# Kernel optimization log

Hardware: AMD Instinct MI355X
Metric: run time of the kernel (lower is better)

The kernel has to match this reference:

```python
import jax, jax.numpy as jnp
import numpy as np

B, N, NE = 16, 96, 256
ATOM, EDIM, HID, LAT, HEADS = 128, 16, 128, 128, 4
HD = LAT // HEADS
RBF, CUT, ZEMB, MAXZ = 16, 5.0, 32, 100
MUL0_IN, MUL1_IN = 64, 32      # irreps_node = 64x0e + 32x1o (dim 160)
MUL0_OUT, MUL1_OUT = 32, 16    # out irreps  = 32x0e + 16x1o (dim 80)
NODE_DIM = MUL0_IN + 3 * MUL1_IN
OUT_DIM = MUL0_OUT + 3 * MUL1_OUT
E_ATT = 1024
WNUM = MUL0_IN*MUL0_OUT + MUL0_IN*MUL1_OUT + MUL1_IN*MUL1_OUT + MUL1_IN*MUL0_OUT  # 4608


def _mlp3(x, w1, b1, w2, b2, w3, b3):
    x = jax.nn.silu(x @ w1 + b1)
    x = jax.nn.silu(x @ w2 + b2)
    return x @ w3 + b3


def setup_inputs() -> dict:
    key = jax.random.key(0)
    ks = jax.random.split(key, 40)
    s = 0.05  # scale params so deep MLP activations stay numerically sane
    d = {}
    d['h'] = jax.random.normal(ks[0], (B, N, ATOM), jnp.float32)
    d['h_full'] = jax.random.normal(ks[1], (B, N, NODE_DIM), jnp.float32)
    d['e_feat'] = jax.random.normal(ks[2], (NE, EDIM), jnp.float32)
    d['att_dist'] = jax.random.uniform(ks[3], (E_ATT,), jnp.float32)
    d['att_vec'] = jax.random.normal(ks[4], (E_ATT, 3), jnp.float32)
    d['z_emb_table'] = jax.random.normal(ks[5], (MAXZ + 1, ZEMB), jnp.float32) * s
    d['rw1'] = jax.random.normal(ks[6], (ZEMB + 1 + RBF, HID), jnp.float32) * s
    d['rb1'] = jnp.zeros((HID,), jnp.float32)
    d['rw2'] = jax.random.normal(ks[7], (HID, WNUM), jnp.float32) * s
    d['rb2'] = jnp.zeros((WNUM,), jnp.float32)
    d['ew1'] = jax.random.normal(ks[8], (EDIM, HID), jnp.float32) * s
    d['eb1'] = jnp.zeros((HID,), jnp.float32)
    d['ew2'] = jax.random.normal(ks[9], (HID, MUL0_OUT + MUL1_OUT), jnp.float32) * s
    d['eb2'] = jnp.zeros((MUL0_OUT + MUL1_OUT,), jnp.float32)
    d['qw1'] = jax.random.normal(ks[10], (ATOM + EDIM, HID), jnp.float32) * s
    d['qb1'] = jnp.zeros((HID,), jnp.float32)
    d['qw2'] = jax.random.normal(ks[11], (HID, HID), jnp.float32) * s
    d['qb2'] = jnp.zeros((HID,), jnp.float32)
    d['qw3'] = jax.random.normal(ks[12], (HID, LAT), jnp.float32) * s
    d['qb3'] = jnp.zeros((LAT,), jnp.float32)
    d['kw1'] = jax.random.normal(ks[13], (ATOM + ZEMB + 1 + RBF, HID), jnp.float32) * s
    d['kb1'] = jnp.zeros((HID,), jnp.float32)
    d['kw2'] = jax.random.normal(ks[14], (HID, HID), jnp.float32) * s
    d['kb2'] = jnp.zeros((HID,), jnp.float32)
    d['kw3'] = jax.random.normal(ks[15], (HID, LAT), jnp.float32) * s
    d['kb3'] = jnp.zeros((LAT,), jnp.float32)
    d['ow1'] = jax.random.normal(ks[16], (MUL0_OUT + MUL1_OUT, HID), jnp.float32) * s
    d['ob1'] = jnp.zeros((HID,), jnp.float32)
    d['ow2'] = jax.random.normal(ks[17], (HID, HID), jnp.float32) * s
    d['ob2'] = jnp.zeros((HID,), jnp.float32)
    d['ow3'] = jax.random.normal(ks[18], (HID, LAT), jnp.float32) * s
    d['ob3'] = jnp.zeros((LAT,), jnp.float32)
    d['z'] = jax.random.randint(ks[19], (B, N), 0, MAXZ)
    d['mask'] = jnp.ones((B, N), bool)
    d['absorber_index'] = jax.random.randint(ks[20], (B,), 0, N)
    d['att_dst'] = jnp.arange(E_ATT)  # unique flat indices into B*N
    return d


def reference(h, h_full, e_feat, att_dist, att_vec, z_emb_table,
              rw1, rb1, rw2, rb2, ew1, eb1, ew2, eb2,
              qw1, qb1, qw2, qb2, qw3, qb3,
              kw1, kb1, kw2, kb2, kw3, kb3,
              ow1, ob1, ow2, ob2, ow3, ob3,
              z, mask, absorber_index, att_dst):
    Bz, Na, Hd = h.shape
    F = Bz * Na
    nE = e_feat.shape[0]
    # scatter edge data into flat (B*N) atom slots
    am_flat = jnp.zeros((F,), bool).at[att_dst].set(True)
    d_flat = jnp.zeros((F,), h.dtype).at[att_dst].set(att_dist)
    v_flat = jnp.zeros((F, 3), h.dtype).at[att_dst].set(att_vec)
    att_mask = am_flat.reshape(Bz, Na) & mask
    # spherical harmonics (lmax=1, component normalization): Y0 = 1, Y1 = sqrt(3)*unit_vec
    un = v_flat / jnp.maximum(jnp.linalg.norm(v_flat, axis=-1, keepdims=True), 1e-8)
    y1 = jnp.sqrt(3.0) * un
    # Gaussian RBF on absorber->atom distance
    mu = jnp.linspace(0.0, CUT, RBF)
    delta = CUT / (RBF - 1)
    rbf = jnp.exp(-(d_flat[:, None] - mu) ** 2 / (2.0 * delta * delta))  # (F, RBF)
    zr = z_emb_table[z]                      # (B, N, ZEMB)
    zr_flat = zr.reshape(F, -1)
    is_abs = jnp.zeros((Bz, Na), h.dtype).at[jnp.arange(Bz), absorber_index].set(1.0)
    # radial MLP -> per-edge tensor-product weights
    w_in = jnp.concatenate([zr_flat, is_abs.reshape(F, 1), rbf], -1)
    tpw = jax.nn.silu(w_in @ rw1 + rb1) @ rw2 + rb2  # (F, WNUM)
    s1 = MUL0_IN * MUL0_OUT
    s2 = s1 + MUL0_IN * MUL1_OUT
    s3 = s2 + MUL1_IN * MUL1_OUT
    w00 = tpw[:, :s1].reshape(F, MUL0_IN, MUL0_OUT)   # 0e x 0e -> 0e
    w01 = tpw[:, s1:s2].reshape(F, MUL0_IN, MUL1_OUT) # 0e x 1o -> 1o
    w10 = tpw[:, s2:s3].reshape(F, MUL1_IN, MUL1_OUT) # 1o x 0e -> 1o
    w11 = tpw[:, s3:].reshape(F, MUL1_IN, MUL0_OUT)   # 1o x 1o -> 0e
    hf = h_full.reshape(F, -1)
    x0 = hf[:, :MUL0_IN]
    x1 = hf[:, MUL0_IN:].reshape(F, MUL1_IN, 3)
    alpha = 1.0 / jnp.sqrt(jnp.float32(MUL0_IN + MUL1_IN))  # path fan-in normalization
    c = 1.0 / jnp.sqrt(3.0)                                  # wigner-3j coeff for l=1 couplings
    out0 = alpha * (jnp.einsum('fi,fio->fo', x0, w00)
                    + c * jnp.einsum('fim,fm,fio->fo', x1, y1, w11))
    out1 = alpha * c * (jnp.einsum('fi,fm,fio->fom', x0, y1, w01)
                        + jnp.einsum('fim,fio->fom', x1, w10))
    v_irrep = jnp.concatenate([out0, out1.reshape(F, 3 * MUL1_OUT)], -1)  # (F, OUT_DIM)
    # cosine cutoff envelope + edge mask
    env = jnp.where(d_flat < CUT, 0.5 * (jnp.cos(jnp.pi * d_flat / CUT) + 1.0), 0.0)
    v_irrep = v_irrep * (am_flat.astype(h.dtype) * env)[:, None]
    # energy-conditioned per-irrep-channel modulation
    gates = jax.nn.silu(e_feat @ ew1 + eb1) @ ew2 + eb2  # (nE, 48)
    g_exp = jnp.concatenate([gates[:, :MUL0_OUT],
                             jnp.repeat(gates[:, MUL0_OUT:], 3, axis=-1)], -1)  # (nE, OUT_DIM)
    v_mod = (v_irrep[:, None, :] * g_exp[None]).reshape(Bz, Na, nE, OUT_DIM)
    # invariant multi-head scoring
    h_abs = h[jnp.arange(Bz), absorber_index]  # (B, H)
    q_in = jnp.concatenate([jnp.broadcast_to(h_abs[:, None], (Bz, nE, Hd)),
                            jnp.broadcast_to(e_feat[None], (Bz, nE, EDIM))], -1)
    q = _mlp3(q_in, qw1, qb1, qw2, qb2, qw3, qb3)  # (B, nE, LAT)
    atom_static = jnp.concatenate([h, zr, is_abs[..., None], rbf.reshape(Bz, Na, RBF)], -1)
    k = _mlp3(atom_static, kw1, kb1, kw2, kb2, kw3, kb3)  # (B, N, LAT)
    qh = q.reshape(Bz, nE, HEADS, HD)
    kh = k.reshape(Bz, Na, HEADS, HD)
    scores = (jnp.einsum('behd,bnhd->benh', qh, kh) * (HD ** -0.5)).mean(-1)  # (B, nE, N)
    m = att_mask[:, None, :]
    scores = jnp.where(m, scores, -1e9)
    attn = jax.nn.softmax(scores, axis=2) * m.astype(h.dtype)
    attn = attn / jnp.maximum(attn.sum(2, keepdims=True), 1e-8)
    out_irrep = jnp.einsum('ben,bnec->bec', attn, v_mod)  # (B, nE, OUT_DIM)
    # invariants: scalars + vector norms
    scal = out_irrep[..., :MUL0_OUT]
    vec = out_irrep[..., MUL0_OUT:].reshape(Bz, nE, MUL1_OUT, 3)
    inv = jnp.concatenate([scal, jnp.sqrt(jnp.sum(vec * vec, -1) + 1e-12)], -1)
    return _mlp3(inv, ow1, ob1, ow2, ob2, ow3, ob3)  # (B, nE, LAT)
```

## Files before the change

kernel.cpp:

```cpp
#include <hip/hip_runtime.h>
#include <hip/hip_fp16.h>
#include <math.h>

#define BB 16
#define NN 96
#define NE 256
#define FF (BB*NN)
#define ATOM 128
#define EDIM 16
#define HID 128
#define LAT 128
#define RBFN 16
#define CUTOFF 5.0f
#define ZEMB 32
#define E_ATT 1024
#define M0I 64
#define M1I 32
#define M0O 32
#define M1O 16
#define NODE_DIM 160
#define OUT_DIM 80
#define INVD 48
#define WNUM 4608
#define SEG1 2048
#define SEG2 3072
#define SEG3 3584

#define NODE_BLKS (FF/4)
#define EC_BLKS 16
#define HABS_BLKS 2
#define GATE_BLKS 16
#define STAGE1_BLKS (NODE_BLKS + EC_BLKS + HABS_BLKS + GATE_BLKS)

#define MFMA_BLKS (36*16)
#define MQ_BLKS (MFMA_BLKS + 512)

typedef _Float16 half8_t __attribute__((ext_vector_type(8)));
typedef float float4v __attribute__((ext_vector_type(4)));

__device__ __forceinline__ float silu_f(float x) { return x / (1.0f + expf(-x)); }

__global__ __launch_bounds__(256) void k_prep(
    const float* __restrict__ rw2,
    const int* __restrict__ att_dst, const float* __restrict__ att_dist,
    const float* __restrict__ att_vec,
    __half* __restrict__ rw2T, int* __restrict__ inv,
    float* __restrict__ y1E, float* __restrict__ envE)
{
    int blk = blockIdx.x;
    int t = threadIdx.x;
    if (blk < 144) {
        __shared__ __half lds[64][66];
        int nt = blk % 72, kt = blk / 72;
        int n0 = nt*64, k0 = kt*64;
        for (int p = 0; p < 16; p++) {
            int idx = t + 256*p;
            int kk = idx >> 6, nn = idx & 63;
            lds[nn][kk] = __float2half(rw2[(k0+kk)*WNUM + n0+nn]);
        }
        __syncthreads();
        for (int p = 0; p < 16; p++) {
            int idx = t + 256*p;
            int nn = idx >> 6, kk = idx & 63;
            rw2T[(n0+nn)*HID + k0+kk] = lds[nn][kk];
        }
        return;
    }
    for (int p = 0; p < 6; p++) inv[t + 256*p] = -1;
    for (int p = 0; p < 4; p++) {
        int e = t + 256*p;
        float d = att_dist[e];
        envE[e] = (d < CUTOFF) ? 0.5f*(cosf(3.14159265358979323846f*d/CUTOFF) + 1.0f) : 0.0f;
        float vx = att_vec[3*e], vy = att_vec[3*e+1], vz = att_vec[3*e+2];
        float nrm = sqrtf(vx*vx + vy*vy + vz*vz);
        float is = 1.0f / fmaxf(nrm, 1e-8f);
        const float s3 = 1.7320508075688772f;
        y1E[3*e]   = s3*vx*is;
        y1E[3*e+1] = s3*vy*is;
        y1E[3*e+2] = s3*vz*is;
    }
    __syncthreads();
    for (int p = 0; p < 4; p++) { int e = t + 256*p; inv[att_dst[e]] = e; }
}

__global__ __launch_bounds__(256) void k_stage1(
    const float* __restrict__ h, const float* __restrict__ z_emb, const int* __restrict__ z,
    const int* __restrict__ absorber, const float* __restrict__ e_feat,
    const int* __restrict__ inv, const float* __restrict__ att_dist,
    const float* __restrict__ rw1, const float* __restrict__ rb1,
    const float* __restrict__ kw1, const float* __restrict__ kb1,
    const float* __restrict__ kw2, const float* __restrict__ kb2,
    const float* __restrict__ kw3, const float* __restrict__ kb3,
    const float* __restrict__ qw1,
    const float* __restrict__ ew1, const float* __restrict__ eb1,
    const float* __restrict__ ew2, const float* __restrict__ eb2,
    __half* __restrict__ hiddenH, float* __restrict__ kmatw,
    float* __restrict__ ecw, float* __restrict__ habs1w, float* __restrict__ gexp)
{
    __shared__ float smem[3488];
    int blk = blockIdx.x;
    int t = threadIdx.x;

    if (blk < NODE_BLKS) {
        float (*sin1)[184] = (float(*)[184])smem;
        float (*l1S)[128]  = (float(*)[128])(smem + 736);
        float (*l2S)[128]  = (float(*)[128])(smem + 736 + 512);
        int f0 = blk * 4;
        {
            int n = t >> 6, i2 = t & 63;
            float2 hv = *(const float2*)&h[(f0 + n)*ATOM + i2*2];
            sin1[n][i2*2] = hv.x; sin1[n][i2*2 + 1] = hv.y;
        }
        if (t < 128) {
            int n = t >> 5, j = t & 31;
            sin1[n][ATOM + j] = z_emb[z[f0 + n]*ZEMB + j];
        }
        if (t < 64) {
            int n = t >> 4, j = t & 15;
            int e = inv[f0 + n];
            float d = ((unsigned)e < E_ATT) ? att_dist[e] : 0.0f;
            const float delta = CUTOFF / (RBFN - 1);
            float diff = d - j*delta;
            sin1[n][ATOM + ZEMB + 1 + j] = expf(-diff*diff / (2.0f*delta*delta));
        }
        if (t < 4) {
            int f = f0 + t;
            int b = f / NN, nn = f - b*NN;
            sin1[t][ATOM + ZEMB] = (absorber[b] == nn) ? 1.0f : 0.0f;
        }
        __syncthreads();
        int n = t >> 6;
        int c2 = (t & 63) * 2;
        int e = inv[f0 + n];
        bool att_ = ((unsigned)e < E_ATT);
        if (att_) {
            float2 a0 = *(const float2*)&rb1[c2];
            float2 a1 = make_float2(0.f, 0.f);
            #pragma unroll 8
            for (int i = 0; i < 48; i += 2) {
                float x0v = sin1[n][ATOM + i], x1v = sin1[n][ATOM + i + 1];
                float2 w0 = *(const float2*)&rw1[i*HID + c2];
                float2 w1 = *(const float2*)&rw1[(i+1)*HID + c2];
                a0.x += x0v*w0.x; a0.y += x0v*w0.y;
                a1.x += x1v*w1.x; a1.y += x1v*w1.y;
            }
            {
                float x0v = sin1[n][ATOM + 48];
                float2 w0 = *(const float2*)&rw1[48*HID + c2];
                a0.x += x0v*w0.x; a0.y += x0v*w0.y;
            }
            *(__half2*)&hiddenH[e*HID + c2] =
                __floats2half2_rn(silu_f(a0.x + a1.x), silu_f(a0.y + a1.y));
        }
        {
            float2 a0 = *(const float2*)&kb1[c2];
            float2 a1 = make_float2(0.f, 0.f);
            #pragma unroll 8
            for (int i = 0; i < 176; i += 2) {
                float x0v = sin1[n][i], x1v = sin1[n][i + 1];
                float2 w0 = *(const float2*)&kw1[i*HID + c2];
                float2 w1 = *(const float2*)&kw1[(i+1)*HID + c2];
                a0.x += x0v*w0.x; a0.y += x0v*w0.y;
                a1.x += x1v*w1.x; a1.y += x1v*w1.y;
            }
            {
                float x0v = sin1[n][176];
                float2 w0 = *(const float2*)&kw1[176*HID + c2];
                a0.x += x0v*w0.x; a0.y += x0v*w0.y;
            }
            l1S[n][c2] = silu_f(a0.x + a1.x); l1S[n][c2+1] = silu_f(a0.y + a1.y);
        }
        __syncthreads();
        {
            float2 a0 = *(const float2*)&kb2[c2];
            float2 a1 = make_float2(0.f, 0.f);
            #pragma unroll 8
            for (int i = 0; i < HID; i += 2) {
                float x0v = l1S[n][i], x1v = l1S[n][i + 1];
                float2 w0 = *(const float2*)&kw2[i*HID + c2];
                float2 w1 = *(const float2*)&kw2[(i+1)*HID + c2];
                a0.x += x0v*w0.x; a0.y += x0v*w0.y;
                a1.x += x1v*w1.x; a1.y += x1v*w1.y;
            }
            l2S[n][c2] = silu_f(a0.x + a1.x); l2S[n][c2+1] = silu_f(a0.y + a1.y);
        }
        __syncthreads();
        {
            float2 a0 = *(const float2*)&kb3[c2];
            float2 a1 = make_float2(0.f, 0.f);
            #pragma unroll 8
            for (int i = 0; i < HID; i += 2) {
                float x0v = l2S[n][i], x1v = l2S[n][i + 1];
                float2 w0 = *(const float2*)&kw3[i*HID + c2];
                float2 w1 = *(const float2*)&kw3[(i+1)*HID + c2];
                a0.x += x0v*w0.x; a0.y += x0v*w0.y;
                a1.x += x1v*w1.x; a1.y += x1v*w1.y;
            }
            float2 o; o.x = a0.x + a1.x; o.y = a0.y + a1.y;
            *(float2*)&kmatw[(f0 + n)*HID + c2] = o;
        }
    } else if (blk < NODE_BLKS + EC_BLKS) {
        float (*ef)[16] = (float(*)[16])smem;
        int e0 = (blk - NODE_BLKS) * 16;
        { int e = t >> 4, i = t & 15; ef[e][i] = e_feat[(e0 + e)*EDIM + i]; }
        __syncthreads();
        int r = t >> 4, c0 = (t & 15)*8;
        float4 a0 = make_float4(0,0,0,0), a1 = a0;
        #pragma unroll
        for (int i = 0; i < EDIM; i++) {
            float a = ef[r][i];
            float4 w0 = *(const float4*)&qw1[(ATOM + i)*HID + c0];
            float4 w1 = *(const float4*)&qw1[(ATOM + i)*HID + c0 + 4];
            a0.x += a*w0.x; a0.y += a*w0.y; a0.z += a*w0.z; a0.w += a*w0.w;
            a1.x += a*w1.x; a1.y += a*w1.y; a1.z += a*w1.z; a1.w += a*w1.w;
        }
        *(float4*)&ecw[(e0 + r)*HID + c0] = a0;
        *(float4*)&ecw[(e0 + r)*HID + c0 + 4] = a1;
    } else if (blk < NODE_BLKS + EC_BLKS + HABS_BLKS) {
        float (*hr)[128] = (float(*)[128])smem;
        int b0 = (blk - NODE_BLKS - EC_BLKS) * 8;
        {
            int r = t >> 5, i4 = t & 31;
            int b = b0 + r;
            int a = absorber[b];
            *(float4*)&hr[r][i4*4] = *(const float4*)&h[(b*NN + a)*ATOM + i4*4];
        }
        __syncthreads();
        int r = t >> 5, c0 = (t & 31)*4;
        float4 a0 = make_float4(0,0,0,0), a1 = a0;
        #pragma unroll 8
        for (int i = 0; i < ATOM; i += 2) {
            float x0v = hr[r][i], x1v = hr[r][i+1];
            float4 w0 = *(const float4*)&qw1[i*HID + c0];
            float4 w1 = *(const float4*)&qw1[(i+1)*HID + c0];
            a0.x += x0v*w0.x; a0.y += x0v*w0.y; a0.z += x0v*w0.z; a0.w += x0v*w0.w;
            a1.x += x1v*w1.x; a1.y += x1v*w1.y; a1.z += x1v*w1.z; a1.w += x1v*w1.w;
        }
        float4 o;
        o.x = a0.x + a1.x; o.y = a0.y + a1.y; o.z = a0.z + a1.z; o.w = a0.w + a1.w;
        *(float4*)&habs1w[(b0 + r)*HID + c0] = o;
    } else {
        float (*ef)[16]   = (float(*)[16])smem;
        float (*l1g)[128] = (float(*)[128])(smem + 256);
        float (*gg)[48]   = (float(*)[48])(smem + 256 + 2048);
        int e0 = (blk - NODE_BLKS - EC_BLKS - HABS_BLKS) * 16;
        { int e = t >> 4, i = t & 15; ef[e][i] = e_feat[(e0 + e)*EDIM + i]; }
        __syncthreads();
        int r = t >> 4, c0 = (t & 15)*8;
        {
            float4 a0 = *(const float4*)&eb1[c0];
            float4 a1 = *(const float4*)&eb1[c0 + 4];
            #pragma unroll
            for (int i = 0; i < EDIM; i++) {
                float a = ef[r][i];
                float4 w0 = *(const float4*)&ew1[i*HID + c0];
                float4 w1 = *(const float4*)&ew1[i*HID + c0 + 4];
                a0.x += a*w0.x; a0.y += a*w0.y; a0.z += a*w0.z; a0.w += a*w0.w;
                a1.x += a*w1.x; a1.y += a*w1.y; a1.z += a*w1.z; a1.w += a*w1.w;
            }
            l1g[r][c0]   = silu_f(a0.x); l1g[r][c0+1] = silu_f(a0.y);
            l1g[r][c0+2] = silu_f(a0.z); l1g[r][c0+3] = silu_f(a0.w);
            l1g[r][c0+4] = silu_f(a1.x); l1g[r][c0+5] = silu_f(a1.y);
            l1g[r][c0+6] = silu_f(a1.z); l1g[r][c0+7] = silu_f(a1.w);
        }
        __syncthreads();
        for (int u = t; u < 16*48; u += 256) {
            int e = u / 48, j = u - 48*(u/48);
            float acc = eb2[j];
            #pragma unroll 4
            for (int i = 0; i < HID; i++) acc += l1g[e][i]*ew2[i*48 + j];
            gg[e][j] = acc;
        }
        __syncthreads();
        for (int u = t; u < 16*80; u += 256) {
            int e = u / 80, cc = u - 80*(u/80);
            gexp[(e0 + e)*OUT_DIM + cc] = (cc < M0O) ? gg[e][cc] : gg[e][M0O + (cc - M0O)/3];
        }
    }
}

__global__ __launch_bounds__(256) void k_mq(
    const __half* __restrict__ hiddenH, const __half* __restrict__ rw2T,
    const float* __restrict__ rb2,
    const float* __restrict__ habs1, const float* __restrict__ ec, const float* __restrict__ qb1,
    const float* __restrict__ qw2, const float* __restrict__ qb2,
    const float* __restrict__ qw3, const float* __restrict__ qb3,
    __half* __restrict__ tpwE, float* __restrict__ qmat)
{
    __shared__ float smem[2048];
    int blk = blockIdx.x;
    int t = threadIdx.x;
    if (blk < MFMA_BLKS) {
        int colTile = blk % 36;
        int rowGrp  = blk / 36;
        int wv = t >> 6;
        int lane = t & 63;
        int m0 = (rowGrp*4 + wv) * 16;
        int n0 = colTile * 128;
        int mrow = lane & 15, quad = lane >> 4;
        const _Float16* hp = (const _Float16*)hiddenH + (m0 + mrow)*HID + quad*8;
        half8_t af[4];
        #pragma unroll
        for (int kc = 0; kc < 4; kc++) af[kc] = *(const half8_t*)(hp + kc*32);
        #pragma unroll
        for (int nt = 0; nt < 8; nt++) {
            const _Float16* bp = (const _Float16*)rw2T + (n0 + nt*16 + mrow)*HID + quad*8;
            float4v acc = {0.f, 0.f, 0.f, 0.f};
            #pragma unroll
            for (int kc = 0; kc < 4; kc++) {
                half8_t bf = *(const half8_t*)(bp + kc*32);
                acc = __builtin_amdgcn_mfma_f32_16x16x32_f16(af[kc], bf, acc, 0, 0, 0);
            }
            int col = n0 + nt*16 + mrow;
            float bias = rb2[col];
            int rbase = m0 + quad*4;
            #pragma unroll
            for (int r = 0; r < 4; r++)
                tpwE[(long)(rbase + r)*WNUM + col] = __float2half(acc[r] + bias);
        }
    } else {
        float* l1S = smem;
        float* l2S = smem + 1024;
        int r0 = (blk - MFMA_BLKS) * 8;
        for (int p = 0; p < 4; p++) {
            int idx = t + 256*p;
            int rr = idx >> 7, i = idx & 127;
            int be = r0 + rr; int b = be >> 8; int e = be & 255;
            l1S[rr*128 + i] = silu_f(habs1[b*HID + i] + ec[e*HID + i] + qb1[i]);
        }
        __syncthreads();
        int r = t >> 5, c0 = (t & 31)*4;
        {
            float4 a0 = *(const float4*)&qb2[c0];
            float4 a1 = make_float4(0,0,0,0);
            #pragma unroll 8
            for (int i = 0; i < HID; i += 2) {
                float x0v = l1S[r*128 + i], x1v = l1S[r*128 + i+1];
                float4 w0 = *(const float4*)&qw2[i*HID + c0];
                float4 w1 = *(const float4*)&qw2[(i+1)*HID + c0];
                a0.x += x0v*w0.x; a0.y += x0v*w0.y; a0.z += x0v*w0.z; a0.w += x0v*w0.w;
                a1.x += x1v*w1.x; a1.y += x1v*w1.y; a1.z += x1v*w1.z; a1.w += x1v*w1.w;
            }
            l2S[r*128 + c0]   = silu_f(a0.x + a1.x); l2S[r*128 + c0+1] = silu_f(a0.y + a1.y);
            l2S[r*128 + c0+2] = silu_f(a0.z + a1.z); l2S[r*128 + c0+3] = silu_f(a0.w + a1.w);
        }
        __syncthreads();
        {
            float4 a0 = *(const float4*)&qb3[c0];
            float4 a1 = make_float4(0,0,0,0);
            #pragma unroll 8
            for (int i = 0; i < HID; i += 2) {
                float x0v = l2S[r*128 + i], x1v = l2S[r*128 + i+1];
                float4 w0 = *(const float4*)&qw3[i*HID + c0];
                float4 w1 = *(const float4*)&qw3[(i+1)*HID + c0];
                a0.x += x0v*w0.x; a0.y += x0v*w0.y; a0.z += x0v*w0.z; a0.w += x0v*w0.w;
                a1.x += x1v*w1.x; a1.y += x1v*w1.y; a1.z += x1v*w1.z; a1.w += x1v*w1.w;
            }
            float4 o;
            o.x = a0.x + a1.x; o.y = a0.y + a1.y; o.z = a0.z + a1.z; o.w = a0.w + a1.w;
            *(float4*)&qmat[(r0 + r)*LAT + c0] = o;
        }
    }
}

__global__ __launch_bounds__(256) void k_score(
    const float* __restrict__ qmat, const float* __restrict__ kmat, const int* __restrict__ inv,
    float* __restrict__ scoresW)
{
    int b  = blockIdx.x >> 3;
    int e0 = (blockIdx.x & 7) * 32;
    int t = threadIdx.x;
    __shared__ float Qs[32][132];
    __shared__ float Ks[96][132];
    __shared__ float mS[NN];

    for (int p = 0; p < 4; p++) {
        int idx = t + 256*p; int e = idx >> 5, i4 = idx & 31;
        *(float4*)&Qs[e][i4*4] = *(const float4*)&qmat[(b*NE + e0 + e)*LAT + i4*4];
    }
    for (int p = 0; p < 12; p++) {
        int idx = t + 256*p; int n = idx >> 5, i4 = idx & 31;
        *(float4*)&Ks[n][i4*4] = *(const float4*)&kmat[(b*NN + n)*LAT + i4*4];
    }
    if (t < NN) mS[t] = ((unsigned)inv[b*NN + t] < E_ATT) ? 1.0f : 0.0f;
    __syncthreads();

    int te = t >> 5;
    int tn = t & 31;
    float acc[4][3] = {};
    for (int i = 0; i < LAT; i++) {
        float bv0 = Ks[tn][i], bv1 = Ks[tn + 32][i], bv2 = Ks[tn + 64][i];
        #pragma unroll
        for (int j = 0; j < 4; j++) {
            float a = Qs[te*4 + j][i];
            acc[j][0] += a*bv0; acc[j][1] += a*bv1; acc[j][2] += a*bv2;
        }
    }
    const float scale = 0.04419417382415922f;
    #pragma unroll
    for (int j = 0; j < 4; j++)
        #pragma unroll
        for (int jj = 0; jj < 3; jj++) {
            int n = tn + 32*jj;
            float s = (mS[n] != 0.f) ? acc[j][jj]*scale : -1e9f;
            scoresW[((b*NE) + e0 + te*4 + j)*NN + n] = s;
        }
}

__global__ __launch_bounds__(256) void k_attf(
    const float* __restrict__ scoresW, const int* __restrict__ inv,
    const float* __restrict__ virr, const float* __restrict__ gexp,
    const float* __restrict__ ow1, const float* __restrict__ ob1,
    const float* __restrict__ ow2, const float* __restrict__ ob2,
    const float* __restrict__ ow3, const float* __restrict__ ob3,
    float* __restrict__ out)
{
    int b  = blockIdx.x >> 5;
    int e0 = (blockIdx.x & 31) * 8;
    int t = threadIdx.x;
    __shared__ float aS[8][100];
    __shared__ float gS[8][84];
    __shared__ float ocS[8][84];
    __shared__ float mS[NN];
    __shared__ float inS[8][INVD];
    __shared__ float l1S[8][HID];
    __shared__ float l2S[8][HID];

    for (int p = 0; p < 3; p++) {
        int idx = t + 256*p;
        int el = idx / NN, n = idx - NN*(idx/NN);
        aS[el][n] = scoresW[((b*NE) + e0 + el)*NN + n];
    }
    if (t < 160) {
        int el = t / 20, c4 = t - 20*(t/20);
        *(float4*)&gS[el][c4*4] = *(const float4*)&gexp[(e0 + el)*OUT_DIM + c4*4];
    }
    if (t < NN) mS[t] = ((unsigned)inv[b*NN + t] < E_ATT) ? 1.0f : 0.0f;
    __syncthreads();

    {
        int el = t >> 5;
        int ng = t & 31;
        float s0 = aS[el][ng], s1 = aS[el][ng + 32], s2 = aS[el][ng + 64];
        float m0 = mS[ng], m1 = mS[ng + 32], m2 = mS[ng + 64];
        float mx = fmaxf(s0, fmaxf(s1, s2));
        #pragma unroll
        for (int off = 1; off < 32; off <<= 1) mx = fmaxf(mx, __shfl_xor(mx, off));
        float e0v = expf(s0 - mx), e1v = expf(s1 - mx), e2v = expf(s2 - mx);
        float sm = e0v + e1v + e2v;
        #pragma unroll
        for (int off = 1; off < 32; off <<= 1) sm += __shfl_xor(sm, off);
        float r = 1.0f / sm;
        float p0 = m0*e0v*r, p1 = m1*e1v*r, p2 = m2*e2v*r;
        float ss = p0 + p1 + p2;
        #pragma unroll
        for (int off = 1; off < 32; off <<= 1) ss += __shfl_xor(ss, off);
        float is = 1.0f / fmaxf(ss, 1e-8f);
        aS[el][ng]      = p0*is;
        aS[el][ng + 32] = p1*is;
        aS[el][ng + 64] = p2*is;
    }
    __syncthreads();

    if (t < 160) {
        int el = t / 20, c4 = t - 20*(t/20);
        const float* vp = virr + (long)b*NN*OUT_DIM + c4*4;
        float4 acc = make_float4(0,0,0,0);
        #pragma unroll 4
        for (int n = 0; n < NN; n++) {
            float a = aS[el][n];
            float4 v = *(const float4*)&vp[n*OUT_DIM];
            acc.x += a*v.x; acc.y += a*v.y; acc.z += a*v.z; acc.w += a*v.w;
        }
        float4 g = *(float4*)&gS[el][c4*4];
        float4 o; o.x = acc.x*g.x; o.y = acc.y*g.y; o.z = acc.z*g.z; o.w = acc.w*g.w;
        *(float4*)&ocS[el][c4*4] = o;
    }
    __syncthreads();

    for (int u = t; u < 8*INVD; u += 256) {
        int el = u / INVD, j = u - INVD*(u/INVD);
        float val;
        if (j < M0O) val = ocS[el][j];
        else {
            int o = j - M0O;
            float x = ocS[el][M0O + 3*o], y = ocS[el][M0O + 3*o + 1], zz = ocS[el][M0O + 3*o + 2];
            val = sqrtf(x*x + y*y + zz*zz + 1e-12f);
        }
        inS[el][j] = val;
    }
    __syncthreads();

    int r = t >> 5, c0 = (t & 31)*4;
    {
        float4 a0 = *(const float4*)&ob1[c0];
        float4 a1 = make_float4(0,0,0,0);
        #pragma unroll 8
        for (int i = 0; i < INVD; i += 2) {
            float x0v = inS[r][i], x1v = inS[r][i+1];
            float4 w0 = *(const float4*)&ow1[i*HID + c0];
            float4 w1 = *(const float4*)&ow1[(i+1)*HID + c0];
            a0.x += x0v*w0.x; a0.y += x0v*w0.y; a0.z += x0v*w0.z; a0.w += x0v*w0.w;
            a1.x += x1v*w1.x; a1.y += x1v*w1.y; a1.z += x1v*w1.z; a1.w += x1v*w1.w;
        }
        l1S[r][c0]   = silu_f(a0.x + a1.x); l1S[r][c0+1] = silu_f(a0.y + a1.y);
        l1S[r][c0+2] = silu_f(a0.z + a1.z); l1S[r][c0+3] = silu_f(a0.w + a1.w);
    }
    __syncthreads();
    {
        float4 a0 = *(const float4*)&ob2[c0];
        float4 a1 = make_float4(0,0,0,0);
        #pragma unroll 8
        for (int i = 0; i < HID; i += 2) {
            float x0v = l1S[r][i], x1v = l1S[r][i+1];
            float4 w0 = *(const float4*)&ow2[i*HID + c0];
            float4 w1 = *(const float4*)&ow2[(i+1)*HID + c0];
            a0.x += x0v*w0.x; a0.y += x0v*w0.y; a0.z += x0v*w0.z; a0.w += x0v*w0.w;
            a1.x += x1v*w1.x; a1.y += x1v*w1.y; a1.z += x1v*w1.z; a1.w += x1v*w1.w;
        }
        l2S[r][c0]   = silu_f(a0.x + a1.x); l2S[r][c0+1] = silu_f(a0.y + a1.y);
        l2S[r][c0+2] = silu_f(a0.z + a1.z); l2S[r][c0+3] = silu_f(a0.w + a1.w);
    }
    __syncthreads();
    {
        float4 a0 = *(const float4*)&ob3[c0];
        float4 a1 = make_float4(0,0,0,0);
        #pragma unroll 8
        for (int i = 0; i < HID; i += 2) {
            float x0v = l2S[r][i], x1v = l2S[r][i+1];
            float4 w0 = *(const float4*)&ow3[i*HID + c0];
            float4 w1 = *(const float4*)&ow3[(i+1)*HID + c0];
            a0.x += x0v*w0.x; a0.y += x0v*w0.y; a0.z += x0v*w0.z; a0.w += x0v*w0.w;
            a1.x += x1v*w1.x; a1.y += x1v*w1.y; a1.z += x1v*w1.z; a1.w += x1v*w1.w;
        }
        float4 o;
        o.x = a0.x + a1.x; o.y = a0.y + a1.y; o.z = a0.z + a1.z; o.w = a0.w + a1.w;
        *(float4*)&out[((b*NE + e0) + r)*LAT + c0] = o;
    }
}

__global__ __launch_bounds__(128) void k_tp(
    const float* __restrict__ h_full, const __half* __restrict__ tpwE,
    const int* __restrict__ att_dst,
    const float* __restrict__ envE, const float* __restrict__ y1E,
    float* __restrict__ virr)
{
    int e = blockIdx.x; int t = threadIdx.x;
    int f = att_dst[e];
    __shared__ float x0[M0I];
    __shared__ float x1f[M1I*3];
    __shared__ float xy[M1I];
    __shared__ float y1s[3];
    const float* hf = h_full + f*NODE_DIM;
    if (t < M0I) x0[t] = hf[t];
    if (t < M1I*3) x1f[t] = hf[M0I + t];
    if (t < 3) y1s[t] = y1E[3*e + t];
    __syncthreads();
    if (t < M1I) xy[t] = x1f[3*t]*y1s[0] + x1f[3*t+1]*y1s[1] + x1f[3*t+2]*y1s[2];
    __syncthreads();
    float scale = envE[e];
    const __half* w = tpwE + (long)e*WNUM;
    const float alpha = 0.10206207261596575f;
    const float cc = 0.5773502691896258f;
    if (t < M0O) {
        float t00 = 0.f, t11 = 0.f;
        #pragma unroll 4
        for (int i = 0; i < M0I; i++) t00 += x0[i]*__half2float(w[i*M0O + t]);
        #pragma unroll 4
        for (int i = 0; i < M1I; i++) t11 += xy[i]*__half2float(w[SEG3 + i*M0O + t]);
        virr[f*OUT_DIM + t] = alpha*(t00 + cc*t11)*scale;
    } else if (t < M0O + 3*M1O) {
        int idx = t - M0O; int o = idx/3, m = idx - 3*o;
        float t01 = 0.f, t10 = 0.f;
        #pragma unroll 4
        for (int i = 0; i < M0I; i++) t01 += x0[i]*__half2float(w[SEG1 + i*M1O + o]);
        #pragma unroll 4
        for (int i = 0; i < M1I; i++) t10 += x1f[i*3 + m]*__half2float(w[SEG2 + i*M1O + o]);
        virr[f*OUT_DIM + t] = alpha*cc*(t01*y1s[m] + t10)*scale;
    }
}

extern "C" void kernel_launch(void* const* d_in, const int* in_sizes, int n_in,
                              void* d_out, int out_size, void* d_ws, size_t ws_size,
                              hipStream_t stream) {
    const float* h        = (const float*)d_in[0];
    const float* h_full   = (const float*)d_in[1];
    const float* e_feat   = (const float*)d_in[2];
    const float* att_dist = (const float*)d_in[3];
    const float* att_vec  = (const float*)d_in[4];
    const float* z_emb    = (const float*)d_in[5];
    const float* rw1 = (const float*)d_in[6];  const float* rb1 = (const float*)d_in[7];
    const float* rw2 = (const float*)d_in[8];  const float* rb2 = (const float*)d_in[9];
    const float* ew1 = (const float*)d_in[10]; const float* eb1 = (const float*)d_in[11];
    const float* ew2 = (const float*)d_in[12]; const float* eb2 = (const float*)d_in[13];
    const float* qw1 = (const float*)d_in[14]; const float* qb1 = (const float*)d_in[15];
    const float* qw2 = (const float*)d_in[16]; const float* qb2 = (const float*)d_in[17];
    const float* qw3 = (const float*)d_in[18]; const float* qb3 = (const float*)d_in[19];
    const float* kw1 = (const float*)d_in[20]; const float* kb1 = (const float*)d_in[21];
    const float* kw2 = (const float*)d_in[22]; const float* kb2 = (const float*)d_in[23];
    const float* kw3 = (const float*)d_in[24]; const float* kb3 = (const float*)d_in[25];
    const float* ow1 = (const float*)d_in[26]; const float* ob1 = (const float*)d_in[27];
    const float* ow2 = (const float*)d_in[28]; const float* ob2 = (const float*)d_in[29];
    const float* ow3 = (const float*)d_in[30]; const float* ob3 = (const float*)d_in[31];
    const int* z        = (const int*)d_in[32];
    const int* absorber = (const int*)d_in[34];
    const int* att_dst  = (const int*)d_in[35];

    float* ws = (float*)d_ws;
    int*   inv     = (int*)ws;
    float* y1E     = ws + 1536;
    float* envE    = ws + 4608;
    float* kmat    = ws + 5632;
    float* qmat    = ws + 202240;
    float* gexp    = ws + 726528;
    float* virr    = ws + 747008;
    float* habs1   = ws + 869888;
    float* ec      = ws + 871936;
    float* scoresW = ws + 904704;
    __half* tpwE   = (__half*)(ws + 1297920);
    __half* rw2T   = (__half*)(ws + 3657216);
    __half* hiddenH= (__half*)(ws + 3952128);

    float* out = (float*)d_out;

    k_prep<<<145, 256, 0, stream>>>(rw2, att_dst, att_dist, att_vec, rw2T, inv, y1E, envE);
    k_stage1<<<STAGE1_BLKS, 256, 0, stream>>>(h, z_emb, z, absorber, e_feat, inv, att_dist,
                                              rw1, rb1, kw1, kb1, kw2, kb2, kw3, kb3,
                                              qw1, ew1, eb1, ew2, eb2,
                                              hiddenH, kmat, ec, habs1, gexp);
    k_mq<<<MQ_BLKS, 256, 0, stream>>>(hiddenH, rw2T, rb2, habs1, ec, qb1,
                                      qw2, qb2, qw3, qb3, tpwE, qmat);
    k_score<<<128, 256, 0, stream>>>(qmat, kmat, inv, scoresW);
    k_tp<<<E_ATT, 128, 0, stream>>>(h_full, tpwE, att_dst, envE, y1E, virr);
    k_attf<<<BB*32, 256, 0, stream>>>(scoresW, inv, virr, gexp,
                                      ow1, ob1, ow2, ob2, ow3, ob3, out);
}
```

Baseline: 250.5 us.

## Move rw2 transpose into stage1, stage MFMA output via LDS, pack tp blocks

The rw2 fp16 transpose moves out of k_prep into extra blocks of k_stage1, so it runs alongside the node MLP work. k_prep shrinks to a single 1024-thread block. The MFMA epilogue in k_mq now stages each 16x128 tile in LDS and writes tpwE rows as 16-byte vectors instead of scattered 2-byte stores. k_tp processes two edges per 256-thread block. Together these aim to cut launch and serialization overhead and uncoalesced global writes, at the cost of more LDS use in k_mq.

Result: no change. 248.4 us (-0.8%).

```diff
diff --git a/kernel.cpp b/kernel.cpp
--- a/kernel.cpp
+++ b/kernel.cpp
@@ -30,7 +30,8 @@
 #define EC_BLKS 16
 #define HABS_BLKS 2
 #define GATE_BLKS 16
-#define STAGE1_BLKS (NODE_BLKS + EC_BLKS + HABS_BLKS + GATE_BLKS)
+#define TRANS_BLKS 144
+#define STAGE1_BLKS (NODE_BLKS + EC_BLKS + HABS_BLKS + GATE_BLKS + TRANS_BLKS)
 
 #define MFMA_BLKS (36*16)
 #define MQ_BLKS (MFMA_BLKS + 512)
@@ -40,47 +41,27 @@
 
 __device__ __forceinline__ float silu_f(float x) { return x / (1.0f + expf(-x)); }
 
-__global__ __launch_bounds__(256) void k_prep(
-    const float* __restrict__ rw2,
+__global__ __launch_bounds__(1024) void k_prep(
     const int* __restrict__ att_dst, const float* __restrict__ att_dist,
     const float* __restrict__ att_vec,
-    __half* __restrict__ rw2T, int* __restrict__ inv,
-    float* __restrict__ y1E, float* __restrict__ envE)
+    int* __restrict__ inv, float* __restrict__ y1E, float* __restrict__ envE)
 {
-    int blk = blockIdx.x;
     int t = threadIdx.x;
-    if (blk < 144) {
-        __shared__ __half lds[64][66];
-        int nt = blk % 72, kt = blk / 72;
-        int n0 = nt*64, k0 = kt*64;
-        for (int p = 0; p < 16; p++) {
-            int idx = t + 256*p;
-            int kk = idx >> 6, nn = idx & 63;
-            lds[nn][kk] = __float2half(rw2[(k0+kk)*WNUM + n0+nn]);
-        }
-        __syncthreads();
-        for (int p = 0; p < 16; p++) {
-            int idx = t + 256*p;
-            int nn = idx >> 6, kk = idx & 63;
-            rw2T[(n0+nn)*HID + k0+kk] = lds[nn][kk];
-        }
-        return;
-    }
-    for (int p = 0; p < 6; p++) inv[t + 256*p] = -1;
-    for (int p = 0; p < 4; p++) {
-        int e = t + 256*p;
-        float d = att_dist[e];
-        envE[e] = (d < CUTOFF) ? 0.5f*(cosf(3.14159265358979323846f*d/CUTOFF) + 1.0f) : 0.0f;
-        float vx = att_vec[3*e], vy = att_vec[3*e+1], vz = att_vec[3*e+2];
+    inv[t] = -1;
+    if (t < FF - 1024) inv[1024 + t] = -1;
+    {
+        float d = att_dist[t];
+        envE[t] = (d < CUTOFF) ? 0.5f*(cosf(3.14159265358979323846f*d/CUTOFF) + 1.0f) : 0.0f;
+        float vx = att_vec[3*t], vy = att_vec[3*t+1], vz = att_vec[3*t+2];
         float nrm = sqrtf(vx*vx + vy*vy + vz*vz);
         float is = 1.0f / fmaxf(nrm, 1e-8f);
         const float s3 = 1.7320508075688772f;
-        y1E[3*e]   = s3*vx*is;
-        y1E[3*e+1] = s3*vy*is;
-        y1E[3*e+2] = s3*vz*is;
-    }
-    __syncthreads();
-    for (int p = 0; p < 4; p++) { int e = t + 256*p; inv[att_dst[e]] = e; }
+        y1E[3*t]   = s3*vx*is;
+        y1E[3*t+1] = s3*vy*is;
+        y1E[3*t+2] = s3*vz*is;
+    }
+    __syncthreads();
+    inv[att_dst[t]] = t;
 }
 
 __global__ __launch_bounds__(256) void k_stage1(
@@ -94,8 +75,10 @@
     const float* __restrict__ qw1,
     const float* __restrict__ ew1, const float* __restrict__ eb1,
     const float* __restrict__ ew2, const float* __restrict__ eb2,
+    const float* __restrict__ rw2,
     __half* __restrict__ hiddenH, float* __restrict__ kmatw,
-    float* __restrict__ ecw, float* __restrict__ habs1w, float* __restrict__ gexp)
+    float* __restrict__ ecw, float* __restrict__ habs1w, float* __restrict__ gexp,
+    __half* __restrict__ rw2T)
 {
     __shared__ float smem[3488];
     int blk = blockIdx.x;
@@ -239,7 +222,7 @@
         float4 o;
         o.x = a0.x + a1.x; o.y = a0.y + a1.y; o.z = a0.z + a1.z; o.w = a0.w + a1.w;
         *(float4*)&habs1w[(b0 + r)*HID + c0] = o;
-    } else {
+    } else if (blk < NODE_BLKS + EC_BLKS + HABS_BLKS + GATE_BLKS) {
         float (*ef)[16]   = (float(*)[16])smem;
         float (*l1g)[128] = (float(*)[128])(smem + 256);
         float (*gg)[48]   = (float(*)[48])(smem + 256 + 2048);
@@ -276,6 +259,22 @@
             int e = u / 80, cc = u - 80*(u/80);
             gexp[(e0 + e)*OUT_DIM + cc] = (cc < M0O) ? gg[e][cc] : gg[e][M0O + (cc - M0O)/3];
         }
+    } else {
+        __half* lds = (__half*)smem;
+        int tb = blk - (NODE_BLKS + EC_BLKS + HABS_BLKS + GATE_BLKS);
+        int nt = tb % 72, kt = tb / 72;
+        int n0 = nt*64, k0 = kt*64;
+        for (int p = 0; p < 16; p++) {
+            int idx = t + 256*p;
+            int kk = idx >> 6, nn = idx & 63;
+            lds[nn*66 + kk] = __float2half(rw2[(k0+kk)*WNUM + n0+nn]);
+        }
+        __syncthreads();
+        for (int p = 0; p < 16; p++) {
+            int idx = t + 256*p;
+            int nn = idx >> 6, kk = idx & 63;
+            rw2T[(n0+nn)*HID + k0+kk] = lds[nn*66 + kk];
+        }
     }
 }
 
@@ -287,7 +286,7 @@
     const float* __restrict__ qw3, const float* __restrict__ qb3,
     __half* __restrict__ tpwE, float* __restrict__ qmat)
 {
-    __shared__ float smem[2048];
+    __shared__ __align__(16) char smemraw[17408];
     int blk = blockIdx.x;
     int t = threadIdx.x;
     if (blk < MFMA_BLKS) {
@@ -298,6 +297,7 @@
         int m0 = (rowGrp*4 + wv) * 16;
         int n0 = colTile * 128;
         int mrow = lane & 15, quad = lane >> 4;
+        __half* cS = (__half*)smemraw + wv * (16*136);
         const _Float16* hp = (const _Float16*)hiddenH + (m0 + mrow)*HID + quad*8;
         half8_t af[4];
         #pragma unroll
@@ -311,16 +311,21 @@
                 half8_t bf = *(const half8_t*)(bp + kc*32);
                 acc = __builtin_amdgcn_mfma_f32_16x16x32_f16(af[kc], bf, acc, 0, 0, 0);
             }
-            int col = n0 + nt*16 + mrow;
-            float bias = rb2[col];
-            int rbase = m0 + quad*4;
+            float bias = rb2[n0 + nt*16 + mrow];
             #pragma unroll
             for (int r = 0; r < 4; r++)
-                tpwE[(long)(rbase + r)*WNUM + col] = __float2half(acc[r] + bias);
+                cS[(quad*4 + r)*136 + nt*16 + mrow] = __float2half(acc[r] + bias);
+        }
+        #pragma unroll
+        for (int p = 0; p < 4; p++) {
+            int chunk = lane + 64*p;
+            int row = chunk >> 4, c8 = (chunk & 15)*8;
+            float4 v = *(float4*)&cS[row*136 + c8];
+            *(float4*)&tpwE[(long)(m0 + row)*WNUM + n0 + c8] = v;
         }
     } else {
-        float* l1S = smem;
-        float* l2S = smem + 1024;
+        float* l1S = (float*)smemraw;
+        float* l2S = (float*)smemraw + 1024;
         int r0 = (blk - MFMA_BLKS) * 8;
         for (int p = 0; p < 4; p++) {
             int idx = t + 256*p;
@@ -405,6 +410,50 @@
             float s = (mS[n] != 0.f) ? acc[j][jj]*scale : -1e9f;
             scoresW[((b*NE) + e0 + te*4 + j)*NN + n] = s;
         }
+}
+
+__global__ __launch_bounds__(256) void k_tp(
+    const float* __restrict__ h_full, const __half* __restrict__ tpwE,
+    const int* __restrict__ att_dst,
+    const float* __restrict__ envE, const float* __restrict__ y1E,
+    float* __restrict__ virr)
+{
+    int t = threadIdx.x;
+    int sub = t >> 7, tt = t & 127;
+    int e = blockIdx.x*2 + sub;
+    int f = att_dst[e];
+    __shared__ float x0[2][M0I];
+    __shared__ float x1f[2][M1I*3];
+    __shared__ float xy[2][M1I];
+    __shared__ float y1s[2][3];
+    const float* hf = h_full + f*NODE_DIM;
+    if (tt < M0I) x0[sub][tt] = hf[tt];
+    if (tt < M1I*3) x1f[sub][tt] = hf[M0I + tt];
+    if (tt < 3) y1s[sub][tt] = y1E[3*e + tt];
+    __syncthreads();
+    if (tt < M1I) xy[sub][tt] = x1f[sub][3*tt]*y1s[sub][0] + x1f[sub][3*tt+1]*y1s[sub][1]
+                              + x1f[sub][3*tt+2]*y1s[sub][2];
+    __syncthreads();
+    float scale = envE[e];
+    const __half* w = tpwE + (long)e*WNUM;
+    const float alpha = 0.10206207261596575f;
+    const float cc = 0.5773502691896258f;
+    if (tt < M0O) {
+        float t00 = 0.f, t11 = 0.f;
+        #pragma unroll 4
+        for (int i = 0; i < M0I; i++) t00 += x0[sub][i]*__half2float(w[i*M0O + tt]);
+        #pragma unroll 4
+        for (int i = 0; i < M1I; i++) t11 += xy[sub][i]*__half2float(w[SEG3 + i*M0O + tt]);
+        virr[f*OUT_DIM + tt] = alpha*(t00 + cc*t11)*scale;
+    } else if (tt < M0O + 3*M1O) {
+        int idx = tt - M0O; int o = idx/3, m = idx - 3*o;
+        float t01 = 0.f, t10 = 0.f;
+        #pragma unroll 4
+        for (int i = 0; i < M0I; i++) t01 += x0[sub][i]*__half2float(w[SEG1 + i*M1O + o]);
+        #pragma unroll 4
+        for (int i = 0; i < M1I; i++) t10 += x1f[sub][i*3 + m]*__half2float(w[SEG2 + i*M1O + o]);
+        virr[f*OUT_DIM + tt] = alpha*cc*(t01*y1s[sub][m] + t10)*scale;
+    }
 }
 
 __global__ __launch_bounds__(256) void k_attf(
@@ -536,47 +585,6 @@
         float4 o;
         o.x = a0.x + a1.x; o.y = a0.y + a1.y; o.z = a0.z + a1.z; o.w = a0.w + a1.w;
         *(float4*)&out[((b*NE + e0) + r)*LAT + c0] = o;
-    }
-}
-
-__global__ __launch_bounds__(128) void k_tp(
-    const float* __restrict__ h_full, const __half* __restrict__ tpwE,
-    const int* __restrict__ att_dst,
-    const float* __restrict__ envE, const float* __restrict__ y1E,
-    float* __restrict__ virr)
-{
-    int e = blockIdx.x; int t = threadIdx.x;
-    int f = att_dst[e];
-    __shared__ float x0[M0I];
-    __shared__ float x1f[M1I*3];
-    __shared__ float xy[M1I];
-    __shared__ float y1s[3];
-    const float* hf = h_full + f*NODE_DIM;
-    if (t < M0I) x0[t] = hf[t];
-    if (t < M1I*3) x1f[t] = hf[M0I + t];
-    if (t < 3) y1s[t] = y1E[3*e + t];
-    __syncthreads();
-    if (t < M1I) xy[t] = x1f[3*t]*y1s[0] + x1f[3*t+1]*y1s[1] + x1f[3*t+2]*y1s[2];
-    __syncthreads();
-    float scale = envE[e];
-    const __half* w = tpwE + (long)e*WNUM;
-    const float alpha = 0.10206207261596575f;
-    const float cc = 0.5773502691896258f;
-    if (t < M0O) {
-        float t00 = 0.f, t11 = 0.f;
-        #pragma unroll 4
-        for (int i = 0; i < M0I; i++) t00 += x0[i]*__half2float(w[i*M0O + t]);
-        #pragma unroll 4
-        for (int i = 0; i < M1I; i++) t11 += xy[i]*__half2float(w[SEG3 + i*M0O + t]);
-        virr[f*OUT_DIM + t] = alpha*(t00 + cc*t11)*scale;
-    } else if (t < M0O + 3*M1O) {
-        int idx = t - M0O; int o = idx/3, m = idx - 3*o;
-        float t01 = 0.f, t10 = 0.f;
-        #pragma unroll 4
-        for (int i = 0; i < M0I; i++) t01 += x0[i]*__half2float(w[SEG1 + i*M1O + o]);
-        #pragma unroll 4
-        for (int i = 0; i < M1I; i++) t10 += x1f[i*3 + m]*__half2float(w[SEG2 + i*M1O + o]);
-        virr[f*OUT_DIM + t] = alpha*cc*(t01*y1s[m] + t10)*scale;
     }
 }
 
@@ -623,15 +631,15 @@
 
     float* out = (float*)d_out;
 
-    k_prep<<<145, 256, 0, stream>>>(rw2, att_dst, att_dist, att_vec, rw2T, inv, y1E, envE);
+    k_prep<<<1, 1024, 0, stream>>>(att_dst, att_dist, att_vec, inv, y1E, envE);
     k_stage1<<<STAGE1_BLKS, 256, 0, stream>>>(h, z_emb, z, absorber, e_feat, inv, att_dist,
                                               rw1, rb1, kw1, kb1, kw2, kb2, kw3, kb3,
-                                              qw1, ew1, eb1, ew2, eb2,
-                                              hiddenH, kmat, ec, habs1, gexp);
+                                              qw1, ew1, eb1, ew2, eb2, rw2,
+                                              hiddenH, kmat, ec, habs1, gexp, rw2T);
     k_mq<<<MQ_BLKS, 256, 0, stream>>>(hiddenH, rw2T, rb2, habs1, ec, qb1,
                                       qw2, qb2, qw3, qb3, tpwE, qmat);
     k_score<<<128, 256, 0, stream>>>(qmat, kmat, inv, scoresW);
-    k_tp<<<E_ATT, 128, 0, stream>>>(h_full, tpwE, att_dst, envE, y1E, virr);
+    k_tp<<<E_ATT/2, 256, 0, stream>>>(h_full, tpwE, att_dst, envE, y1E, virr);
     k_attf<<<BB*32, 256, 0, stream>>>(scoresW, inv, virr, gexp,
                                       ow1, ob1, ow2, ob2, ow3, ob3, out);
 }
```
